# Kernel tuning notes

Measured on AMD Instinct MI355X. Metric: run time of the kernel, lower is better.

## Reference

```python
import jax, jax.numpy as jnp
import numpy as np


def _conv1x1(x, w, b=None):
    # x: (N,C,H,W), w: (O,C) -> (N,O,H,W)
    y = jnp.einsum('nchw,oc->nohw', x, w)
    return y if b is None else y + b[None, :, None, None]


def _norm(f):
    # per-channel zero-mean / unit-std over (N,H,W); torch.std is unbiased (ddof=1)
    mean = f.mean(axis=(0, 2, 3), keepdims=True)
    std = f.std(axis=(0, 2, 3), ddof=1, keepdims=True)
    return (f - mean) / (std + 1e-6)


def _causal_attention(x, w_cls):
    N, C, H, W = x.shape
    M = _conv1x1(x, w_cls).reshape(N, -1, H * W)     # (N,K,HW)
    sm = jax.nn.softmax(M, axis=2)                   # softmax over spatial
    return jnp.einsum('nkp,ncp->nkc', sm, x.reshape(N, C, H * W))  # (N,K,C)


def _ccnet(x, wq, bq, wk, bk, wv, bv, gamma1):
    B, C, H, W = x.shape
    q = _conv1x1(x, wq, bq)  # (B,Cq,H,W)
    k = _conv1x1(x, wk, bk)
    v = _conv1x1(x, wv, bv)  # (B,C,H,W)
    # column (vertical) attention energies with -inf on the self diagonal
    eH = jnp.einsum('bciw,bcjw->biwj', q, k)         # (B,H,W,H)
    eH = jnp.where(jnp.eye(H, dtype=bool)[None, :, None, :], -jnp.inf, eH)
    # row (horizontal) attention energies
    eW = jnp.einsum('bchi,bchj->bhij', q, k)         # (B,H,W,W)
    att = jax.nn.softmax(jnp.concatenate([eH, eW], axis=3), axis=3)
    attH, attW = att[..., :H], att[..., H:]
    outH = jnp.einsum('bcjw,biwj->bciw', v, attH)    # aggregate along column
    outW = jnp.einsum('bchj,bhij->bchi', v, attW)    # aggregate along row
    return gamma1 * (outH + outW) + x


def setup_inputs() -> dict:
    key = jax.random.key(0)
    ks = jax.random.split(key, 10)
    B, C, H, W = 8, 256, 96, 96
    Cq, K = C // 8, 6
    f32 = jnp.float32
    return {
        'preds_S': jax.random.normal(ks[0], (B, C, H, W), f32),
        'preds_T': jax.random.normal(ks[1], (B, C, H, W), f32),
        'w_cls': jax.random.normal(ks[2], (K, C), f32) * 0.05,
        'wq': jax.random.normal(ks[3], (Cq, C), f32) * 0.05,
        'bq': jnp.zeros((Cq,), f32),
        'wk': jax.random.normal(ks[4], (Cq, C), f32) * 0.05,
        'bk': jnp.zeros((Cq,), f32),
        'wv': jax.random.normal(ks[5], (C, C), f32) * 0.05,
        'bv': jnp.zeros((C,), f32),
        'gamma1': jax.random.normal(ks[6], (1,), f32) * 0.1,
    }


def reference(preds_S, preds_T, w_cls, wq, bq, wk, bk, wv, bv, gamma1):
    CA_W, CC_W = 0.0005, 1e-05
    N = preds_S.shape[0]
    s = _norm(preds_S)
    t = _norm(preds_T)
    ca_t = _causal_attention(t, w_cls)
    ca_s = _causal_attention(s, w_cls)
    ca_loss = jnp.sum((ca_t - ca_s) ** 2) / N
    cc_t = _ccnet(t, wq, bq, wk, bk, wv, bv, gamma1)
    cc_s = _ccnet(s, wq, bq, wk, bk, wv, bv, gamma1)
    cc_loss = jnp.sum((cc_t - cc_s) ** 2) / N
    return ca_loss * CA_W + cc_loss * CC_W
```

## Files before the change

kernel.cpp:

```cpp
#include <hip/hip_runtime.h>
#include <math.h>

#define NBAT 8
#define NC   256
#define NH   96
#define NW   96
#define NP   9216
#define NCQ  32
#define NKC  6
#define NL   192
#define NV   320
#define NTOT 73728

typedef __attribute__((ext_vector_type(4))) float  floatx4;
typedef __attribute__((ext_vector_type(8))) short  short8;

__device__ __forceinline__ float bf2f(unsigned short h){
  return __uint_as_float(((unsigned)h) << 16);
}
__device__ __forceinline__ float bflo(unsigned u){ return __uint_as_float(u << 16); }
__device__ __forceinline__ float bfhi(unsigned u){ return __uint_as_float(u & 0xFFFF0000u); }
__device__ __forceinline__ unsigned short f2bf(float f){
  unsigned u = __float_as_uint(f);
  u += 0x7FFFu + ((u >> 16) & 1u);
  return (unsigned short)(u >> 16);
}

union F4 { float4 v; float a[4]; };

__device__ __forceinline__ float warpReduceSum(float v){
  #pragma unroll
  for (int m = 32; m; m >>= 1) v += __shfl_xor(v, m);
  return v;
}
__device__ __forceinline__ float warpReduceMax(float v){
  #pragma unroll
  for (int m = 32; m; m >>= 1) v = fmaxf(v, __shfl_xor(v, m));
  return v;
}
__device__ float blockReduceSum(float v){
  __shared__ float lds[8];
  v = warpReduceSum(v);
  int wid = threadIdx.x >> 6, lane = threadIdx.x & 63;
  int nw = blockDim.x >> 6;
  if (lane == 0) lds[wid] = v;
  __syncthreads();
  if (wid == 0){
    v = (lane < nw) ? lds[lane] : 0.f;
    #pragma unroll
    for (int m = 4; m; m >>= 1) v += __shfl_xor(v, m);
  }
  __syncthreads();
  return v;
}
__device__ float blockReduceMax(float v){
  __shared__ float lds[8];
  v = warpReduceMax(v);
  int wid = threadIdx.x >> 6, lane = threadIdx.x & 63;
  int nw = blockDim.x >> 6;
  if (lane == 0) lds[wid] = v;
  __syncthreads();
  if (wid == 0){
    v = (lane < nw) ? lds[lane] : -INFINITY;
    #pragma unroll
    for (int m = 4; m; m >>= 1) v = fmaxf(v, __shfl_xor(v, m));
  }
  __syncthreads();
  return v;
}

__global__ __launch_bounds__(256)
void k_stats(const float* __restrict__ S, const float* __restrict__ T,
             float* __restrict__ s_sum, float* __restrict__ s_sq){
  int blk = blockIdx.x;
  int t = blk / (NC * NBAT);
  int rem = blk % (NC * NBAT);
  int c = rem / NBAT;
  int n = rem % NBAT;
  const float4* x4 = (const float4*)((t ? T : S) + ((size_t)n * NC + c) * NP);
  float s = 0.f, q = 0.f;
  for (int p = threadIdx.x; p < NP / 4; p += 256){
    F4 f; f.v = x4[p];
    #pragma unroll
    for (int j = 0; j < 4; j++){ s += f.a[j]; q += f.a[j] * f.a[j]; }
  }
  s = blockReduceSum(s);
  q = blockReduceSum(q);
  if (threadIdx.x == 0){
    atomicAdd(&s_sum[t * NC + c], s);
    atomicAdd(&s_sq[t * NC + c], q);
  }
}

__global__ __launch_bounds__(512)
void k_finalize(const float* __restrict__ s_sum, const float* __restrict__ s_sq,
                float* __restrict__ mean, float* __restrict__ inv){
  int i = threadIdx.x;
  if (i < 2 * NC){
    float s = s_sum[i], q = s_sq[i];
    float m = s / (float)NTOT;
    float var = (q - s * m) / (float)(NTOT - 1);
    var = fmaxf(var, 0.f);
    mean[i] = m;
    inv[i] = 1.f / (sqrtf(var) + 1e-6f);
  }
}

__global__ __launch_bounds__(256)
void k_caM(const float* __restrict__ S, const float* __restrict__ T,
           const float* __restrict__ wcls,
           const float* __restrict__ mean, const float* __restrict__ inv,
           float* __restrict__ smca){
  int pt = blockIdx.x, n = blockIdx.y, t = blockIdx.z;
  __shared__ float wsc[NKC * NC];
  __shared__ float shift[NKC];
  for (int idx = threadIdx.x; idx < NKC * NC; idx += 256){
    int c = idx & 255;
    wsc[idx] = wcls[idx] * inv[t * NC + c];
  }
  __syncthreads();
  if (threadIdx.x < NKC){
    float sh = 0.f;
    for (int c = 0; c < NC; c++) sh += wsc[threadIdx.x * NC + c] * mean[t * NC + c];
    shift[threadIdx.x] = sh;
  }
  __syncthreads();
  int p = pt * 256 + threadIdx.x;
  const float* x = (t ? T : S) + (size_t)n * NC * NP + p;
  float acc[NKC];
  #pragma unroll
  for (int k = 0; k < NKC; k++) acc[k] = 0.f;
  for (int c = 0; c < NC; c++){
    float xv = x[(size_t)c * NP];
    #pragma unroll
    for (int k = 0; k < NKC; k++) acc[k] += wsc[k * NC + c] * xv;
  }
  size_t base = ((size_t)(t * NBAT + n) * NKC) * NP + p;
  #pragma unroll
  for (int k = 0; k < NKC; k++) smca[base + (size_t)k * NP] = acc[k] - shift[k];
}

__global__ __launch_bounds__(256)
void k_caSoftmax(float* __restrict__ smca){
  int r = blockIdx.x;
  float* row = smca + (size_t)r * NP;
  float m = -INFINITY;
  for (int p = threadIdx.x; p < NP; p += 256) m = fmaxf(m, row[p]);
  m = blockReduceMax(m);
  __shared__ float bm, bs;
  if (threadIdx.x == 0) bm = m;
  __syncthreads();
  m = bm;
  float s = 0.f;
  for (int p = threadIdx.x; p < NP; p += 256) s += expf(row[p] - m);
  s = blockReduceSum(s);
  if (threadIdx.x == 0) bs = 1.f / s;
  __syncthreads();
  float rs = bs;
  for (int p = threadIdx.x; p < NP; p += 256) row[p] = expf(row[p] - m) * rs;
}

__global__ __launch_bounds__(256)
void k_caOut(const float* __restrict__ S, const float* __restrict__ T,
             const float* __restrict__ smca,
             const float* __restrict__ mean, const float* __restrict__ inv,
             float* __restrict__ ca){
  int ct = blockIdx.x & 7, ks = blockIdx.x >> 3;
  int n = blockIdx.y, t = blockIdx.z;
  int c0 = ct * 32;
  __shared__ float xt[32 * 264];
  __shared__ float smt[NKC * 256];
  int cl = threadIdx.x >> 3, pl = threadIdx.x & 7;
  float acc[NKC];
  #pragma unroll
  for (int k = 0; k < NKC; k++) acc[k] = 0.f;
  const float* xbase = (t ? T : S) + (size_t)n * NC * NP;
  const float* smbase = smca + (size_t)(t * NBAT + n) * NKC * NP;
  for (int pt = ks * 6; pt < ks * 6 + 6; pt++){
    int p0 = pt * 256;
    for (int idx = threadIdx.x; idx < 32 * 256; idx += 256){
      int r = idx >> 8, p = idx & 255;
      float v = xbase[(size_t)(c0 + r) * NP + p0 + p];
      xt[r * 264 + p] = (v - mean[t * NC + c0 + r]) * inv[t * NC + c0 + r];
    }
    for (int idx = threadIdx.x; idx < NKC * 256; idx += 256){
      int k = idx >> 8, p = idx & 255;
      smt[idx] = smbase[(size_t)k * NP + p0 + p];
    }
    __syncthreads();
    for (int j = 0; j < 32; j++){
      float xv = xt[cl * 264 + pl + 8 * j];
      #pragma unroll
      for (int k = 0; k < NKC; k++) acc[k] += smt[k * 256 + pl + 8 * j] * xv;
    }
    __syncthreads();
  }
  #pragma unroll
  for (int k = 0; k < NKC; k++){
    float v = acc[k];
    v += __shfl_xor(v, 1); v += __shfl_xor(v, 2); v += __shfl_xor(v, 4);
    if (pl == 0) atomicAdd(&ca[((size_t)(t * NBAT + n) * NKC + k) * NC + c0 + cl], v);
  }
}

__global__ __launch_bounds__(256)
void k_caLoss(const float* __restrict__ ca, float* __restrict__ out){
  int i = blockIdx.x * 256 + threadIdx.x;
  float d = 0.f;
  if (i < NBAT * NKC * NC) d = ca[(size_t)NBAT * NKC * NC + i] - ca[i];
  float ss = blockReduceSum(d * d);
  if (threadIdx.x == 0) atomicAdd(out, ss * (0.0005f / 8.0f));
}

__global__ __launch_bounds__(256)
void k_xn(const float* __restrict__ x0, int b0,
          const float* __restrict__ mean, const float* __restrict__ inv, int t,
          unsigned short* __restrict__ XN){
  int pt = blockIdx.x, ct = blockIdx.y, bb = blockIdx.z;
  int bg = b0 + bb;
  int p0 = pt * 64, c0 = ct * 64;
  __shared__ float tile[64 * 65];
  const float* x = x0 + ((size_t)bg * NC + c0) * NP + p0;
  #pragma unroll
  for (int i = 0; i < 4; i++){
    int idx = threadIdx.x + i * 256;
    int r = idx >> 4, g = (idx & 15) * 4;
    F4 f; f.v = *(const float4*)(x + (size_t)r * NP + g);
    float m = mean[t * NC + c0 + r], iv = inv[t * NC + c0 + r];
    #pragma unroll
    for (int j = 0; j < 4; j++) tile[(g + j) * 65 + r] = (f.a[j] - m) * iv;
  }
  __syncthreads();
  #pragma unroll
  for (int i = 0; i < 4; i++){
    int idx = threadIdx.x + i * 256;
    int p = idx >> 4, g = (idx & 15) * 4;
    unsigned lo = (unsigned)f2bf(tile[p * 65 + g + 0]) | ((unsigned)f2bf(tile[p * 65 + g + 1]) << 16);
    unsigned hi = (unsigned)f2bf(tile[p * 65 + g + 2]) | ((unsigned)f2bf(tile[p * 65 + g + 3]) << 16);
    uint2 u; u.x = lo; u.y = hi;
    *(uint2*)(XN + ((size_t)bb * NP + p0 + p) * NC + c0 + g) = u;
  }
}

__global__ __launch_bounds__(256)
void k_wconv(const float* __restrict__ wv, const float* __restrict__ wq,
             const float* __restrict__ wk, unsigned short* __restrict__ Wb){
  int n = blockIdx.x;
  const float* src = (n < 256) ? (wv + (size_t)n * NC)
                   : (n < 288) ? (wq + (size_t)(n - 256) * NC)
                               : (wk + (size_t)(n - 288) * NC);
  Wb[(size_t)n * NC + threadIdx.x] = f2bf(src[threadIdx.x]);
}

__global__ __launch_bounds__(256)
void k_v(const unsigned short* __restrict__ XN, const unsigned short* __restrict__ Wb,
         const float* __restrict__ bv, const float* __restrict__ bq,
         const float* __restrict__ bk,
         unsigned short* __restrict__ VT1,
         unsigned short* __restrict__ qb, unsigned short* __restrict__ kb){
  int pt = blockIdx.x, bb = blockIdx.y;
  int p0 = pt * 64;
  __shared__ unsigned short Wl[NV * 40];
  int lane = threadIdx.x & 63;
  int wid = threadIdx.x >> 6;
  int col = lane & 15, quad = lane >> 4;
  const unsigned short* xnb = XN + (size_t)bb * NP * NC + (size_t)(p0 + wid * 16 + col) * NC;
  floatx4 acc[20];
  #pragma unroll
  for (int nt = 0; nt < 20; nt++) acc[nt] = (floatx4){0.f, 0.f, 0.f, 0.f};

  int ci_n[5], ci_k8[5];
  #pragma unroll
  for (int i = 0; i < 5; i++){ int ci = i * 256 + threadIdx.x; ci_n[i] = ci >> 2; ci_k8[i] = (ci & 3) * 8; }

  short8 w[5];
  #pragma unroll
  for (int i = 0; i < 5; i++)
    w[i] = *(const short8*)(Wb + (size_t)ci_n[i] * NC + ci_k8[i]);

  for (int ks = 0; ks < 8; ks++){
    if (ks) __syncthreads();
    #pragma unroll
    for (int i = 0; i < 5; i++)
      *(short8*)(Wl + ci_n[i] * 40 + ci_k8[i]) = w[i];
    __syncthreads();
    if (ks < 7){
      int k0n = (ks + 1) * 32;
      #pragma unroll
      for (int i = 0; i < 5; i++)
        w[i] = *(const short8*)(Wb + (size_t)ci_n[i] * NC + k0n + ci_k8[i]);
    }
    short8 a = *(const short8*)(xnb + ks * 32 + quad * 8);
    #pragma unroll
    for (int nt = 0; nt < 20; nt++){
      short8 b = *(const short8*)(Wl + (nt * 16 + col) * 40 + quad * 8);
      acc[nt] = __builtin_amdgcn_mfma_f32_16x16x32_bf16(a, b, acc[nt], 0, 0, 0);
    }
  }

  int prow0 = p0 + wid * 16 + quad * 4;
  #pragma unroll
  for (int nt = 0; nt < 16; nt++){
    int c = nt * 16 + col;
    float bias = bv[c];
    uint2 u;
    u.x = (unsigned)f2bf(acc[nt][0] + bias) | ((unsigned)f2bf(acc[nt][1] + bias) << 16);
    u.y = (unsigned)f2bf(acc[nt][2] + bias) | ((unsigned)f2bf(acc[nt][3] + bias) << 16);
    *(uint2*)(VT1 + ((size_t)bb * NC + c) * NP + prow0) = u;
  }
  #pragma unroll
  for (int nt = 16; nt < 18; nt++){
    int c = (nt - 16) * 16 + col;
    float bias = bq[c];
    #pragma unroll
    for (int i = 0; i < 4; i++)
      qb[((size_t)bb * NP + prow0 + i) * NCQ + c] = f2bf(acc[nt][i] + bias);
  }
  #pragma unroll
  for (int nt = 18; nt < 20; nt++){
    int c = (nt - 18) * 16 + col;
    float bias = bk[c];
    #pragma unroll
    for (int i = 0; i < 4; i++)
      kb[((size_t)bb * NP + prow0 + i) * NCQ + c] = f2bf(acc[nt][i] + bias);
  }
}

__global__ __launch_bounds__(256)
void k_vt(const unsigned short* __restrict__ VT1, unsigned short* __restrict__ VT2){
  int c = blockIdx.x, bb = blockIdx.y;
  __shared__ unsigned short tile[96 * 104];
  size_t base = ((size_t)bb * NC + c) * NP;
  for (int idx = threadIdx.x; idx < 1152; idx += 256){
    int h = idx / 12, g = idx % 12;
    short8 v = *(const short8*)(VT1 + base + h * 96 + g * 8);
    #pragma unroll
    for (int kk = 0; kk < 8; kk++) tile[(g * 8 + kk) * 104 + h] = ((unsigned short*)&v)[kk];
  }
  __syncthreads();
  for (int idx = threadIdx.x; idx < 1152; idx += 256){
    int w = idx / 12, g = idx % 12;
    short8 v = *(const short8*)(tile + w * 104 + g * 8);
    *(short8*)(VT2 + base + w * 96 + g * 8) = v;
  }
}

__global__ __launch_bounds__(256)
void k_eH(const unsigned short* __restrict__ qb, const unsigned short* __restrict__ kb,
          unsigned short* __restrict__ att){
  int w = blockIdx.x, bb = blockIdx.y;
  int lane = threadIdx.x & 63, wid = threadIdx.x >> 6;
  int col = lane & 15, quad = lane >> 4;
  int mi0 = (wid & 1) * 3, ni0 = (wid >> 1) * 3;
  short8 a[3], b[3];
  #pragma unroll
  for (int m = 0; m < 3; m++)
    a[m] = *(const short8*)(qb + ((size_t)bb * NP + ((mi0 + m) * 16 + col) * 96 + w) * NCQ + quad * 8);
  #pragma unroll
  for (int n = 0; n < 3; n++)
    b[n] = *(const short8*)(kb + ((size_t)bb * NP + ((ni0 + n) * 16 + col) * 96 + w) * NCQ + quad * 8);
  floatx4 acc[3][3];
  #pragma unroll
  for (int m = 0; m < 3; m++)
    #pragma unroll
    for (int n = 0; n < 3; n++){
      acc[m][n] = (floatx4){0.f, 0.f, 0.f, 0.f};
      acc[m][n] = __builtin_amdgcn_mfma_f32_16x16x32_bf16(a[m], b[n], acc[m][n], 0, 0, 0);
    }
  #pragma unroll
  for (int m = 0; m < 3; m++)
    #pragma unroll
    for (int n = 0; n < 3; n++){
      int j = (ni0 + n) * 16 + col;
      #pragma unroll
      for (int r = 0; r < 4; r++){
        int i = (mi0 + m) * 16 + quad * 4 + r;
        float v = (j == i) ? -INFINITY : acc[m][n][r];
        att[((size_t)bb * NP + i * 96 + w) * NL + j] = f2bf(v);
      }
    }
}

__global__ __launch_bounds__(256)
void k_eW(const unsigned short* __restrict__ qb, const unsigned short* __restrict__ kb,
          unsigned short* __restrict__ att){
  int h = blockIdx.x, bb = blockIdx.y;
  int lane = threadIdx.x & 63, wid = threadIdx.x >> 6;
  int col = lane & 15, quad = lane >> 4;
  int mi0 = (wid & 1) * 3, ni0 = (wid >> 1) * 3;
  short8 a[3], b[3];
  #pragma unroll
  for (int m = 0; m < 3; m++)
    a[m] = *(const short8*)(qb + ((size_t)bb * NP + h * 96 + (mi0 + m) * 16 + col) * NCQ + quad * 8);
  #pragma unroll
  for (int n = 0; n < 3; n++)
    b[n] = *(const short8*)(kb + ((size_t)bb * NP + h * 96 + (ni0 + n) * 16 + col) * NCQ + quad * 8);
  floatx4 acc[3][3];
  #pragma unroll
  for (int m = 0; m < 3; m++)
    #pragma unroll
    for (int n = 0; n < 3; n++){
      acc[m][n] = (floatx4){0.f, 0.f, 0.f, 0.f};
      acc[m][n] = __builtin_amdgcn_mfma_f32_16x16x32_bf16(a[m], b[n], acc[m][n], 0, 0, 0);
    }
  #pragma unroll
  for (int m = 0; m < 3; m++)
    #pragma unroll
    for (int n = 0; n < 3; n++){
      int j = (ni0 + n) * 16 + col;
      #pragma unroll
      for (int r = 0; r < 4; r++){
        int i = (mi0 + m) * 16 + quad * 4 + r;
        att[((size_t)bb * NP + h * 96 + i) * NL + 96 + j] = f2bf(acc[m][n][r]);
      }
    }
}

__global__ __launch_bounds__(256)
void k_attSoftmax(unsigned short* __restrict__ att){
  int q = blockIdx.x * 4 + (threadIdx.x >> 6);
  int lane = threadIdx.x & 63;
  unsigned short* row = att + (size_t)q * NL;
  float e0 = bf2f(row[lane]);
  float e1 = bf2f(row[64 + lane]);
  float e2 = bf2f(row[128 + lane]);
  float m = fmaxf(e0, fmaxf(e1, e2));
  m = warpReduceMax(m);
  float x0 = expf(e0 - m), x1 = expf(e1 - m), x2 = expf(e2 - m);
  float s = warpReduceSum(x0 + x1 + x2);
  float rs = 1.f / s;
  row[lane]       = f2bf(x0 * rs);
  row[64 + lane]  = f2bf(x1 * rs);
  row[128 + lane] = f2bf(x2 * rs);
}

__global__ __launch_bounds__(256)
void k_outH(const unsigned short* __restrict__ VT2, const unsigned short* __restrict__ att,
            unsigned short* __restrict__ OH){
  int w = blockIdx.x, bb = blockIdx.y;
  int lane = threadIdx.x & 63, wid = threadIdx.x >> 6;
  int col = lane & 15, quad = lane >> 4;
  floatx4 acc[6][4];
  #pragma unroll
  for (int m = 0; m < 6; m++)
    #pragma unroll
    for (int n = 0; n < 4; n++) acc[m][n] = (floatx4){0.f, 0.f, 0.f, 0.f};
  #pragma unroll
  for (int ks = 0; ks < 3; ks++){
    int k0 = ks * 32 + quad * 8;
    short8 a[6], b[4];
    #pragma unroll
    for (int m = 0; m < 6; m++)
      a[m] = *(const short8*)(att + ((size_t)bb * NP + (m * 16 + col) * 96 + w) * NL + k0);
    #pragma unroll
    for (int n = 0; n < 4; n++){
      int c = wid * 64 + n * 16 + col;
      b[n] = *(const short8*)(VT2 + ((size_t)bb * NC + c) * NP + w * 96 + k0);
    }
    #pragma unroll
    for (int m = 0; m < 6; m++)
      #pragma unroll
      for (int n = 0; n < 4; n++)
        acc[m][n] = __builtin_amdgcn_mfma_f32_16x16x32_bf16(a[m], b[n], acc[m][n], 0, 0, 0);
  }
  #pragma unroll
  for (int m = 0; m < 6; m++)
    #pragma unroll
    for (int n = 0; n < 4; n++){
      int c = wid * 64 + n * 16 + col;
      #pragma unroll
      for (int r = 0; r < 4; r++){
        int i = m * 16 + quad * 4 + r;
        OH[((size_t)bb * NP + i * 96 + w) * NC + c] = f2bf(acc[m][n][r]);
      }
    }
}

__global__ __launch_bounds__(256)
void k_outW(const unsigned short* __restrict__ VT1, const unsigned short* __restrict__ att,
            const unsigned short* __restrict__ OH, unsigned short* __restrict__ Ot,
            const float* __restrict__ predsS, const float* __restrict__ predsT,
            const float* __restrict__ mean, const float* __restrict__ inv,
            const float* __restrict__ gamma, int b0, int spass,
            float* __restrict__ out){
  int h = blockIdx.x, bb = blockIdx.y;
  int lane = threadIdx.x & 63, wid = threadIdx.x >> 6;
  int col = lane & 15, quad = lane >> 4;
  floatx4 acc[6][4];
  #pragma unroll
  for (int m = 0; m < 6; m++)
    #pragma unroll
    for (int n = 0; n < 4; n++) acc[m][n] = (floatx4){0.f, 0.f, 0.f, 0.f};
  #pragma unroll
  for (int ks = 0; ks < 3; ks++){
    int k0 = ks * 32 + quad * 8;
    short8 a[6], b[4];
    #pragma unroll
    for (int m = 0; m < 6; m++)
      a[m] = *(const short8*)(att + ((size_t)bb * NP + h * 96 + m * 16 + col) * NL + 96 + k0);
    #pragma unroll
    for (int n = 0; n < 4; n++){
      int c = wid * 64 + n * 16 + col;
      b[n] = *(const short8*)(VT1 + ((size_t)bb * NC + c) * NP + h * 96 + k0);
    }
    #pragma unroll
    for (int m = 0; m < 6; m++)
      #pragma unroll
      for (int n = 0; n < 4; n++)
        acc[m][n] = __builtin_amdgcn_mfma_f32_16x16x32_bf16(a[m], b[n], acc[m][n], 0, 0, 0);
  }
  if (!spass){
    #pragma unroll
    for (int m = 0; m < 6; m++)
      #pragma unroll
      for (int n = 0; n < 4; n++){
        int c = wid * 64 + n * 16 + col;
        #pragma unroll
        for (int r = 0; r < 4; r++){
          int i = m * 16 + quad * 4 + r;
          size_t base = ((size_t)bb * NP + h * 96 + i) * NC + c;
          Ot[base] = f2bf(acc[m][n][r] + bf2f(OH[base]));
        }
      }
  } else {
    int bg = b0 + bb;
    float g = gamma[0];
    float ss = 0.f;
    #pragma unroll
    for (int n = 0; n < 4; n++){
      int c = wid * 64 + n * 16 + col;
      float mS = mean[c],      iS = inv[c];
      float mT = mean[NC + c], iT = inv[NC + c];
      const float* tp = predsT + ((size_t)bg * NC + c) * NP + h * 96;
      const float* sp = predsS + ((size_t)bg * NC + c) * NP + h * 96;
      #pragma unroll
      for (int m = 0; m < 6; m++){
        int i0 = m * 16 + quad * 4;
        F4 tv, sv;
        tv.v = *(const float4*)(tp + i0);
        sv.v = *(const float4*)(sp + i0);
        #pragma unroll
        for (int r = 0; r < 4; r++){
          size_t base = ((size_t)bb * NP + h * 96 + i0 + r) * NC + c;
          float os = acc[m][n][r] + bf2f(OH[base]);
          float ot = bf2f(Ot[base]);
          float dn = (tv.a[r] - mT) * iT - (sv.a[r] - mS) * iS;
          float d = g * (ot - os) + dn;
          ss += d * d;
        }
      }
    }
    ss = blockReduceSum(ss);
    if (threadIdx.x == 0) atomicAdd(out, ss * (1e-5f / 8.0f));
  }
}

extern "C" void kernel_launch(void* const* d_in, const int* in_sizes, int n_in,
                              void* d_out, int out_size, void* d_ws, size_t ws_size,
                              hipStream_t stream){
  (void)in_sizes; (void)n_in; (void)out_size;
  const float* S    = (const float*)d_in[0];
  const float* T    = (const float*)d_in[1];
  const float* wcls = (const float*)d_in[2];
  const float* wq   = (const float*)d_in[3];
  const float* bq   = (const float*)d_in[4];
  const float* wk   = (const float*)d_in[5];
  const float* bk   = (const float*)d_in[6];
  const float* wv   = (const float*)d_in[7];
  const float* bv   = (const float*)d_in[8];
  const float* gamma= (const float*)d_in[9];
  float* out = (float*)d_out;

  char* base = (char*)d_ws;
  size_t off = 0;
  auto alloc = [&](size_t b){ size_t o = off; off += (b + 255) & ~(size_t)255; return o; };
  size_t o_ssum = alloc(2 * NC * 4);
  size_t o_ssq  = alloc(2 * NC * 4);
  size_t o_mean = alloc(2 * NC * 4);
  size_t o_inv  = alloc(2 * NC * 4);
  size_t o_wb   = alloc((size_t)NV * NC * 2);
  size_t o_ca   = alloc((size_t)2 * NBAT * NKC * NC * 4);
  size_t o_smca = alloc((size_t)2 * NBAT * NKC * NP * 4);
  size_t fixed = off;
  size_t per_b = (size_t)NP * NC * 2 * 5
               + (size_t)NP * NCQ * 2 * 2
               + (size_t)NP * NL * 2;
  int NB = 8;
  while (NB > 1 && fixed + (size_t)NB * per_b + 8192 > ws_size) NB >>= 1;

  size_t o_xn  = alloc((size_t)NB * NP * NC * 2);
  size_t o_v1  = alloc((size_t)NB * NP * NC * 2);
  size_t o_v2  = alloc((size_t)NB * NP * NC * 2);
  size_t o_q   = alloc((size_t)NB * NP * NCQ * 2);
  size_t o_k   = alloc((size_t)NB * NP * NCQ * 2);
  size_t o_att = alloc((size_t)NB * NP * NL * 2);
  size_t o_oh  = alloc((size_t)NB * NP * NC * 2);
  size_t o_ot  = alloc((size_t)NB * NP * NC * 2);

  float* ssum = (float*)(base + o_ssum);
  float* ssq  = (float*)(base + o_ssq);
  float* mean = (float*)(base + o_mean);
  float* inv  = (float*)(base + o_inv);
  float* ca   = (float*)(base + o_ca);
  float* smca = (float*)(base + o_smca);
  unsigned short* Wb  = (unsigned short*)(base + o_wb);
  unsigned short* XN  = (unsigned short*)(base + o_xn);
  unsigned short* VT1 = (unsigned short*)(base + o_v1);
  unsigned short* VT2 = (unsigned short*)(base + o_v2);
  unsigned short* qbp = (unsigned short*)(base + o_q);
  unsigned short* kbp = (unsigned short*)(base + o_k);
  unsigned short* att = (unsigned short*)(base + o_att);
  unsigned short* OH  = (unsigned short*)(base + o_oh);
  unsigned short* Ot  = (unsigned short*)(base + o_ot);

  hipMemsetAsync(d_out, 0, 4, stream);
  hipMemsetAsync(base + o_ssum, 0, 4096, stream);
  hipMemsetAsync(base + o_ca, 0, (size_t)2 * NBAT * NKC * NC * 4, stream);

  k_stats<<<dim3(2 * NC * NBAT), 256, 0, stream>>>(S, T, ssum, ssq);
  k_finalize<<<1, 512, 0, stream>>>(ssum, ssq, mean, inv);
  k_wconv<<<dim3(NV), 256, 0, stream>>>(wv, wq, wk, Wb);

  k_caM<<<dim3(36, NBAT, 2), 256, 0, stream>>>(S, T, wcls, mean, inv, smca);
  k_caSoftmax<<<dim3(2 * NBAT * NKC), 256, 0, stream>>>(smca);
  k_caOut<<<dim3(48, NBAT, 2), 256, 0, stream>>>(S, T, smca, mean, inv, ca);
  k_caLoss<<<dim3(48), 256, 0, stream>>>(ca, out);

  for (int b0 = 0; b0 < NBAT; b0 += NB){
    for (int pass = 0; pass < 2; pass++){
      int t = (pass == 0) ? 1 : 0;
      const float* x = t ? T : S;
      k_xn<<<dim3(144, 4, NB), 256, 0, stream>>>(x, b0, mean, inv, t, XN);
      k_v<<<dim3(144, NB), 256, 0, stream>>>(XN, Wb, bv, bq, bk, VT1, qbp, kbp);
      k_vt<<<dim3(NC, NB), 256, 0, stream>>>(VT1, VT2);
      k_eH<<<dim3(96, NB), 256, 0, stream>>>(qbp, kbp, att);
      k_eW<<<dim3(96, NB), 256, 0, stream>>>(qbp, kbp, att);
      k_attSoftmax<<<dim3(NB * 2304), 256, 0, stream>>>(att);
      k_outH<<<dim3(96, NB), 256, 0, stream>>>(VT2, att, OH);
      k_outW<<<dim3(96, NB), 256, 0, stream>>>(VT1, att, OH, Ot, S, T, mean, inv,
                                               gamma, b0, pass, out);
    }
  }
}
```

Before: 651.1 us.

## Split outH/outW over channel slices, merge eH/eW launches, alias OH onto XN

Merges the column and row energy kernels into one launch using blockIdx.z to pick the direction. The outH and outW kernels now split the 256 channels across four z-blocks, so each wave computes one 16-channel tile instead of four. That gives 4x more blocks and far fewer accumulator registers, at the cost of reloading the attention rows in every channel slice. The OH buffer now reuses the XN workspace, which is dead after k_v, reducing the per-batch memory footprint so the batch chunk can be larger.

```diff
diff --git a/kernel.cpp b/kernel.cpp
--- a/kernel.cpp
+++ b/kernel.cpp
@@ -346,19 +346,28 @@
 }
 
 __global__ __launch_bounds__(256)
-void k_eH(const unsigned short* __restrict__ qb, const unsigned short* __restrict__ kb,
-          unsigned short* __restrict__ att){
-  int w = blockIdx.x, bb = blockIdx.y;
+void k_e(const unsigned short* __restrict__ qb, const unsigned short* __restrict__ kb,
+         unsigned short* __restrict__ att){
+  int x = blockIdx.x, bb = blockIdx.y, which = blockIdx.z;
   int lane = threadIdx.x & 63, wid = threadIdx.x >> 6;
   int col = lane & 15, quad = lane >> 4;
   int mi0 = (wid & 1) * 3, ni0 = (wid >> 1) * 3;
   short8 a[3], b[3];
-  #pragma unroll
-  for (int m = 0; m < 3; m++)
-    a[m] = *(const short8*)(qb + ((size_t)bb * NP + ((mi0 + m) * 16 + col) * 96 + w) * NCQ + quad * 8);
-  #pragma unroll
-  for (int n = 0; n < 3; n++)
-    b[n] = *(const short8*)(kb + ((size_t)bb * NP + ((ni0 + n) * 16 + col) * 96 + w) * NCQ + quad * 8);
+  if (which == 0){
+    #pragma unroll
+    for (int m = 0; m < 3; m++)
+      a[m] = *(const short8*)(qb + ((size_t)bb * NP + ((mi0 + m) * 16 + col) * 96 + x) * NCQ + quad * 8);
+    #pragma unroll
+    for (int n = 0; n < 3; n++)
+      b[n] = *(const short8*)(kb + ((size_t)bb * NP + ((ni0 + n) * 16 + col) * 96 + x) * NCQ + quad * 8);
+  } else {
+    #pragma unroll
+    for (int m = 0; m < 3; m++)
+      a[m] = *(const short8*)(qb + ((size_t)bb * NP + x * 96 + (mi0 + m) * 16 + col) * NCQ + quad * 8);
+    #pragma unroll
+    for (int n = 0; n < 3; n++)
+      b[n] = *(const short8*)(kb + ((size_t)bb * NP + x * 96 + (ni0 + n) * 16 + col) * NCQ + quad * 8);
+  }
   floatx4 acc[3][3];
   #pragma unroll
   for (int m = 0; m < 3; m++)
@@ -375,43 +384,9 @@
       #pragma unroll
       for (int r = 0; r < 4; r++){
         int i = (mi0 + m) * 16 + quad * 4 + r;
-        float v = (j == i) ? -INFINITY : acc[m][n][r];
-        att[((size_t)bb * NP + i * 96 + w) * NL + j] = f2bf(v);
-      }
-    }
-}
-
-__global__ __launch_bounds__(256)
-void k_eW(const unsigned short* __restrict__ qb, const unsigned short* __restrict__ kb,
-          unsigned short* __restrict__ att){
-  int h = blockIdx.x, bb = blockIdx.y;
-  int lane = threadIdx.x & 63, wid = threadIdx.x >> 6;
-  int col = lane & 15, quad = lane >> 4;
-  int mi0 = (wid & 1) * 3, ni0 = (wid >> 1) * 3;
-  short8 a[3], b[3];
-  #pragma unroll
-  for (int m = 0; m < 3; m++)
-    a[m] = *(const short8*)(qb + ((size_t)bb * NP + h * 96 + (mi0 + m) * 16 + col) * NCQ + quad * 8);
-  #pragma unroll
-  for (int n = 0; n < 3; n++)
-    b[n] = *(const short8*)(kb + ((size_t)bb * NP + h * 96 + (ni0 + n) * 16 + col) * NCQ + quad * 8);
-  floatx4 acc[3][3];
-  #pragma unroll
-  for (int m = 0; m < 3; m++)
-    #pragma unroll
-    for (int n = 0; n < 3; n++){
-      acc[m][n] = (floatx4){0.f, 0.f, 0.f, 0.f};
-      acc[m][n] = __builtin_amdgcn_mfma_f32_16x16x32_bf16(a[m], b[n], acc[m][n], 0, 0, 0);
-    }
-  #pragma unroll
-  for (int m = 0; m < 3; m++)
-    #pragma unroll
-    for (int n = 0; n < 3; n++){
-      int j = (ni0 + n) * 16 + col;
-      #pragma unroll
-      for (int r = 0; r < 4; r++){
-        int i = (mi0 + m) * 16 + quad * 4 + r;
-        att[((size_t)bb * NP + h * 96 + i) * NL + 96 + j] = f2bf(acc[m][n][r]);
+        int p = which ? (x * 96 + i) : (i * 96 + x);
+        float v = (!which && j == i) ? -INFINITY : acc[m][n][r];
+        att[((size_t)bb * NP + p) * NL + (which ? 96 + j : j)] = f2bf(v);
       }
     }
 }
@@ -437,43 +412,33 @@
 __global__ __launch_bounds__(256)
 void k_outH(const unsigned short* __restrict__ VT2, const unsigned short* __restrict__ att,
             unsigned short* __restrict__ OH){
-  int w = blockIdx.x, bb = blockIdx.y;
+  int w = blockIdx.x, bb = blockIdx.y, cs = blockIdx.z;
   int lane = threadIdx.x & 63, wid = threadIdx.x >> 6;
   int col = lane & 15, quad = lane >> 4;
-  floatx4 acc[6][4];
-  #pragma unroll
-  for (int m = 0; m < 6; m++)
-    #pragma unroll
-    for (int n = 0; n < 4; n++) acc[m][n] = (floatx4){0.f, 0.f, 0.f, 0.f};
+  int c = cs * 64 + wid * 16 + col;
+  floatx4 acc[6];
+  #pragma unroll
+  for (int m = 0; m < 6; m++) acc[m] = (floatx4){0.f, 0.f, 0.f, 0.f};
   #pragma unroll
   for (int ks = 0; ks < 3; ks++){
     int k0 = ks * 32 + quad * 8;
-    short8 a[6], b[4];
+    short8 a[6], b;
     #pragma unroll
     for (int m = 0; m < 6; m++)
       a[m] = *(const short8*)(att + ((size_t)bb * NP + (m * 16 + col) * 96 + w) * NL + k0);
-    #pragma unroll
-    for (int n = 0; n < 4; n++){
-      int c = wid * 64 + n * 16 + col;
-      b[n] = *(const short8*)(VT2 + ((size_t)bb * NC + c) * NP + w * 96 + k0);
-    }
+    b = *(const short8*)(VT2 + ((size_t)bb * NC + c) * NP + w * 96 + k0);
     #pragma unroll
     for (int m = 0; m < 6; m++)
-      #pragma unroll
-      for (int n = 0; n < 4; n++)
-        acc[m][n] = __builtin_amdgcn_mfma_f32_16x16x32_bf16(a[m], b[n], acc[m][n], 0, 0, 0);
-  }
-  #pragma unroll
-  for (int m = 0; m < 6; m++)
-    #pragma unroll
-    for (int n = 0; n < 4; n++){
-      int c = wid * 64 + n * 16 + col;
-      #pragma unroll
-      for (int r = 0; r < 4; r++){
-        int i = m * 16 + quad * 4 + r;
-        OH[((size_t)bb * NP + i * 96 + w) * NC + c] = f2bf(acc[m][n][r]);
-      }
-    }
+      acc[m] = __builtin_amdgcn_mfma_f32_16x16x32_bf16(a[m], b, acc[m], 0, 0, 0);
+  }
+  #pragma unroll
+  for (int m = 0; m < 6; m++){
+    #pragma unroll
+    for (int r = 0; r < 4; r++){
+      int i = m * 16 + quad * 4 + r;
+      OH[((size_t)bb * NP + i * 96 + w) * NC + c] = f2bf(acc[m][r]);
+    }
+  }
 }
 
 __global__ __launch_bounds__(256)
@@ -483,71 +448,57 @@
             const float* __restrict__ mean, const float* __restrict__ inv,
             const float* __restrict__ gamma, int b0, int spass,
             float* __restrict__ out){
-  int h = blockIdx.x, bb = blockIdx.y;
+  int h = blockIdx.x, bb = blockIdx.y, cs = blockIdx.z;
   int lane = threadIdx.x & 63, wid = threadIdx.x >> 6;
   int col = lane & 15, quad = lane >> 4;
-  floatx4 acc[6][4];
-  #pragma unroll
-  for (int m = 0; m < 6; m++)
-    #pragma unroll
-    for (int n = 0; n < 4; n++) acc[m][n] = (floatx4){0.f, 0.f, 0.f, 0.f};
+  int c = cs * 64 + wid * 16 + col;
+  floatx4 acc[6];
+  #pragma unroll
+  for (int m = 0; m < 6; m++) acc[m] = (floatx4){0.f, 0.f, 0.f, 0.f};
   #pragma unroll
   for (int ks = 0; ks < 3; ks++){
     int k0 = ks * 32 + quad * 8;
-    short8 a[6], b[4];
+    short8 a[6], b;
     #pragma unroll
     for (int m = 0; m < 6; m++)
       a[m] = *(const short8*)(att + ((size_t)bb * NP + h * 96 + m * 16 + col) * NL + 96 + k0);
-    #pragma unroll
-    for (int n = 0; n < 4; n++){
-      int c = wid * 64 + n * 16 + col;
-      b[n] = *(const short8*)(VT1 + ((size_t)bb * NC + c) * NP + h * 96 + k0);
-    }
+    b = *(const short8*)(VT1 + ((size_t)bb * NC + c) * NP + h * 96 + k0);
     #pragma unroll
     for (int m = 0; m < 6; m++)
+      acc[m] = __builtin_amdgcn_mfma_f32_16x16x32_bf16(a[m], b, acc[m], 0, 0, 0);
+  }
+  if (!spass){
+    #pragma unroll
+    for (int m = 0; m < 6; m++){
       #pragma unroll
-      for (int n = 0; n < 4; n++)
-        acc[m][n] = __builtin_amdgcn_mfma_f32_16x16x32_bf16(a[m], b[n], acc[m][n], 0, 0, 0);
-  }
-  if (!spass){
-    #pragma unroll
-    for (int m = 0; m < 6; m++)
-      #pragma unroll
-      for (int n = 0; n < 4; n++){
-        int c = wid * 64 + n * 16 + col;
-        #pragma unroll
-        for (int r = 0; r < 4; r++){
-          int i = m * 16 + quad * 4 + r;
-          size_t base = ((size_t)bb * NP + h * 96 + i) * NC + c;
-          Ot[base] = f2bf(acc[m][n][r] + bf2f(OH[base]));
-        }
+      for (int r = 0; r < 4; r++){
+        int i = m * 16 + quad * 4 + r;
+        size_t base = ((size_t)bb * NP + h * 96 + i) * NC + c;
+        Ot[base] = f2bf(acc[m][r] + bf2f(OH[base]));
       }
+    }
   } else {
     int bg = b0 + bb;
     float g = gamma[0];
     float ss = 0.f;
-    #pragma unroll
-    for (int n = 0; n < 4; n++){
-      int c = wid * 64 + n * 16 + col;
-      float mS = mean[c],      iS = inv[c];
-      float mT = mean[NC + c], iT = inv[NC + c];
-      const float* tp = predsT + ((size_t)bg * NC + c) * NP + h * 96;
-      const float* sp = predsS + ((size_t)bg * NC + c) * NP + h * 96;
+    float mS = mean[c],      iS = inv[c];
+    float mT = mean[NC + c], iT = inv[NC + c];
+    const float* tp = predsT + ((size_t)bg * NC + c) * NP + h * 96;
+    const float* sp = predsS + ((size_t)bg * NC + c) * NP + h * 96;
+    #pragma unroll
+    for (int m = 0; m < 6; m++){
+      int i0 = m * 16 + quad * 4;
+      F4 tv, sv;
+      tv.v = *(const float4*)(tp + i0);
+      sv.v = *(const float4*)(sp + i0);
       #pragma unroll
-      for (int m = 0; m < 6; m++){
-        int i0 = m * 16 + quad * 4;
-        F4 tv, sv;
-        tv.v = *(const float4*)(tp + i0);
-        sv.v = *(const float4*)(sp + i0);
-        #pragma unroll
-        for (int r = 0; r < 4; r++){
-          size_t base = ((size_t)bb * NP + h * 96 + i0 + r) * NC + c;
-          float os = acc[m][n][r] + bf2f(OH[base]);
-          float ot = bf2f(Ot[base]);
-          float dn = (tv.a[r] - mT) * iT - (sv.a[r] - mS) * iS;
-          float d = g * (ot - os) + dn;
-          ss += d * d;
-        }
+      for (int r = 0; r < 4; r++){
+        size_t base = ((size_t)bb * NP + h * 96 + i0 + r) * NC + c;
+        float os = acc[m][r] + bf2f(OH[base]);
+        float ot = bf2f(Ot[base]);
+        float dn = (tv.a[r] - mT) * iT - (sv.a[r] - mS) * iS;
+        float d = g * (ot - os) + dn;
+        ss += d * d;
       }
     }
     ss = blockReduceSum(ss);
@@ -582,7 +533,7 @@
   size_t o_ca   = alloc((size_t)2 * NBAT * NKC * NC * 4);
   size_t o_smca = alloc((size_t)2 * NBAT * NKC * NP * 4);
   size_t fixed = off;
-  size_t per_b = (size_t)NP * NC * 2 * 5
+  size_t per_b = (size_t)NP * NC * 2 * 4
                + (size_t)NP * NCQ * 2 * 2
                + (size_t)NP * NL * 2;
   int NB = 8;
@@ -594,8 +545,8 @@
   size_t o_q   = alloc((size_t)NB * NP * NCQ * 2);
   size_t o_k   = alloc((size_t)NB * NP * NCQ * 2);
   size_t o_att = alloc((size_t)NB * NP * NL * 2);
-  size_t o_oh  = alloc((size_t)NB * NP * NC * 2);
   size_t o_ot  = alloc((size_t)NB * NP * NC * 2);
+  size_t o_oh  = o_xn;
 
   float* ssum = (float*)(base + o_ssum);
   float* ssq  = (float*)(base + o_ssq);
@@ -633,12 +584,11 @@
       k_xn<<<dim3(144, 4, NB), 256, 0, stream>>>(x, b0, mean, inv, t, XN);
       k_v<<<dim3(144, NB), 256, 0, stream>>>(XN, Wb, bv, bq, bk, VT1, qbp, kbp);
       k_vt<<<dim3(NC, NB), 256, 0, stream>>>(VT1, VT2);
-      k_eH<<<dim3(96, NB), 256, 0, stream>>>(qbp, kbp, att);
-      k_eW<<<dim3(96, NB), 256, 0, stream>>>(qbp, kbp, att);
+      k_e<<<dim3(96, NB, 2), 256, 0, stream>>>(qbp, kbp, att);
       k_attSoftmax<<<dim3(NB * 2304), 256, 0, stream>>>(att);
-      k_outH<<<dim3(96, NB), 256, 0, stream>>>(VT2, att, OH);
-      k_outW<<<dim3(96, NB), 256, 0, stream>>>(VT1, att, OH, Ot, S, T, mean, inv,
-                                               gamma, b0, pass, out);
-    }
-  }
-}
+      k_outH<<<dim3(96, NB, 4), 256, 0, stream>>>(VT2, att, OH);
+      k_outW<<<dim3(96, NB, 4), 256, 0, stream>>>(VT1, att, OH, Ot, S, T, mean, inv,
+                                                  gamma, b0, pass, out);
+    }
+  }
+}
```

Measured after the change: 689.2 us. 1.06x slower.
